# Optimization experiments

Hardware: AMD Instinct MI355X
Metric: run time of the kernel (lower is better)

Reference implementation:

```python
import jax, jax.numpy as jnp
import numpy as np
from jax.scipy.linalg import cho_solve

N = 4096        # num nodes
D = 256         # in_dim == out_dim
NUM_HOPS = 2
R = 32          # subspace_dim
ETA = 0.5
EPS_SUB = 0.5   # eps in coeff = r / (n * eps^2)
LN_EPS = 1e-5


def setup_inputs() -> dict:
    rng = np.random.default_rng(0)
    K = NUM_HOPS + 1
    # sparse-ish binary adjacency mask with self loops
    mask = (rng.random((N, N)) < 0.002).astype(np.float32)
    mask = np.maximum(mask, np.eye(N, dtype=np.float32))
    deg = mask.sum(axis=1, keepdims=True)
    A = (mask / deg).astype(np.float32)          # row-stochastic propagation
    L = (np.eye(N, dtype=np.float32) - A)        # normalized Laplacian
    H = rng.standard_normal((N, D)).astype(np.float32)
    # orthonormal subspace bases per hop, as in __init__ (QR of randn)
    U = np.stack([np.linalg.qr(rng.standard_normal((D, R)))[0][:, :R] for _ in range(K)]).astype(np.float32)
    lambda_laps = np.full((K,), 0.1, dtype=np.float32)
    hop_weights = np.full((K,), 1.0 / K, dtype=np.float32)
    threshold = np.full((D,), 0.05, dtype=np.float32)
    gamma = np.ones((D,), dtype=np.float32)
    beta = np.zeros((D,), dtype=np.float32)
    return {
        "H": jnp.asarray(H), "A": jnp.asarray(A), "adj_mask": jnp.asarray(mask),
        "L": jnp.asarray(L), "U": jnp.asarray(U),
        "lambda_laps": jnp.asarray(lambda_laps), "hop_weights": jnp.asarray(hop_weights),
        "threshold": jnp.asarray(threshold), "gamma": jnp.asarray(gamma), "beta": jnp.asarray(beta),
    }


def reference(H, A, adj_mask, L, U, lambda_laps, hop_weights, threshold, gamma, beta):
    n, d = H.shape
    r = U.shape[-1]
    # multi-hop propagation
    hops = [H]
    Hk = H
    for _ in range(NUM_HOPS):
        Hk = A @ Hk
        hops.append(Hk)
    w = jax.nn.softmax(hop_weights)
    laps = jax.nn.softplus(lambda_laps)
    coeff = r / (n * EPS_SUB ** 2)
    neg = (1.0 - adj_mask) * -1e9
    I_r = jnp.eye(r, dtype=H.dtype)
    agg = jnp.zeros_like(H)        # accumulates grad_k.T, shape [n, d]
    lap_total = jnp.zeros_like(H)
    for k, H_k in enumerate(hops):
        Uk = U[k]                  # [d, r]
        Zk = Uk.T @ H_k.T          # [r, n]
        M = I_r + coeff * (Zk @ Zk.T)              # [r, r], SPD
        Lc = jnp.linalg.cholesky(M)
        M_inv = cho_solve((Lc, True), I_r)         # cholesky_inverse
        MZ = M_inv @ Zk                            # [r, n]
        scores = Zk.T @ MZ + neg                   # [n, n] masked subspace attention
        alpha = jax.nn.softmax(scores, axis=1)
        grad_k = (Uk @ (MZ @ alpha.T)).T           # [n, d]
        agg = agg + w[k] * grad_k
        lap_total = lap_total + laps[k] * (L @ H_k)
    H_half = H + ETA * agg - ETA * lap_total
    # soft-threshold (proj is None since in_dim == out_dim)
    H_out = jnp.sign(H_half) * jax.nn.relu(jnp.abs(H_half) - threshold[None, :])
    H_out = H_out + H              # residual
    mu = H_out.mean(axis=-1, keepdims=True)
    var = H_out.var(axis=-1, keepdims=True)
    H_out = (H_out - mu) / jnp.sqrt(var + LN_EPS) * gamma + beta
    # orthogonality loss over all (k, l) pairs
    K = U.shape[0]
    orth_loss = jnp.asarray(0.0, dtype=H.dtype)
    for k in range(K):
        for l in range(k, K):
            G = U[k].T @ U[l]
            orth_loss = orth_loss + jnp.sum(((G - I_r) if l == k else G) ** 2)
    lap_smooth = jnp.sum(H_out * (L @ H_out))  # trace(H^T L H)
    return H_out, orth_loss, lap_smooth, jax.lax.stop_gradient(w)
```

## Files before the change

### kernel.cpp

```cpp
#include <hip/hip_runtime.h>
#include <math.h>

#define NN 4096
#define DD 256
#define KK 3
#define RR 32
#define MAXNNZ 128

static constexpr float ETA    = 0.5f;
static constexpr float COEFF  = 0.03125f;
static constexpr float LN_EPSF = 1e-5f;

#define OFF_H1   0
#define OFF_H2   (NN*DD)
#define OFF_H3   (2*NN*DD)
#define OFF_Y    (3*NN*DD)
#define OFF_P    (OFF_Y + KK*NN*RR)
#define OFF_M    (OFF_P + KK*NN*RR)
#define OFF_MINV (OFF_M + KK*RR*RR)
#define OFF_SCAL (OFF_MINV + KK*RR*RR)
#define OFF_NNZ  (OFF_SCAL + 8)
#define OFF_COLS (OFF_NNZ + NN)
#define OFF_VALS (OFF_COLS + NN*MAXNNZ)
#define OFF_PART (OFF_VALS + NN*MAXNNZ)
#define OFF_ORTH (OFF_PART + NN/4)
#define OFF_W    (OFF_ORTH + 8)

__global__ __launch_bounds__(256, 4)
void k_csr_prep(const float* __restrict__ A, int* __restrict__ nnz,
                int* __restrict__ cols, float* __restrict__ vals,
                const float* __restrict__ hw, const float* __restrict__ ll,
                const float* __restrict__ U,
                float* __restrict__ ws, float* __restrict__ out,
                const float* __restrict__ H) {
  int b = blockIdx.x;
  int t = threadIdx.x;
  if (b >= NN/2) {
    int p = b - NN/2;
    if (p == 6) {
      if (t == 0) {
        float m = fmaxf(fmaxf(hw[0], hw[1]), hw[2]);
        float e0 = expf(hw[0]-m), e1 = expf(hw[1]-m), e2 = expf(hw[2]-m);
        float s = e0 + e1 + e2;
        float w0 = e0/s, w1 = e1/s, w2 = e2/s;
        ws[OFF_SCAL+0] = w0; ws[OFF_SCAL+1] = w1; ws[OFF_SCAL+2] = w2;
        for (int k = 0; k < KK; ++k) {
          float x = ll[k];
          ws[OFF_SCAL+3+k] = (x > 20.f) ? x : log1pf(expf(x));
        }
        out[NN*DD + 2] = w0; out[NN*DD + 3] = w1; out[NN*DD + 4] = w2;
      }
      for (int idx = t; idx < KK*RR*RR; idx += 256) {
        int rr2 = idx % (RR*RR);
        ws[OFF_M + idx] = ((rr2 / RR) == (rr2 % RR)) ? 1.f : 0.f;
      }
      return;
    }
    int k = (p < 3) ? 0 : ((p < 5) ? 1 : 2);
    int l = (p < 3) ? p : ((p < 5) ? p - 2 : 2);
    int a0 = t >> 5, bb = t & 31;
    float s0 = 0.f, s1 = 0.f, s2 = 0.f, s3 = 0.f;
    for (int dd = 0; dd < DD; ++dd) {
      float ul = U[(size_t)l*DD*RR + dd*RR + bb];
      const float* uk = U + (size_t)k*DD*RR + dd*RR;
      s0 += uk[a0]      * ul;
      s1 += uk[a0 + 8]  * ul;
      s2 += uk[a0 + 16] * ul;
      s3 += uk[a0 + 24] * ul;
    }
    if (k == l && bb == a0)      s0 -= 1.f;
    if (k == l && bb == a0 + 8)  s1 -= 1.f;
    if (k == l && bb == a0 + 16) s2 -= 1.f;
    if (k == l && bb == a0 + 24) s3 -= 1.f;
    float sq = s0*s0 + s1*s1 + s2*s2 + s3*s3;
    #pragma unroll
    for (int o = 32; o > 0; o >>= 1) sq += __shfl_xor(sq, o, 64);
    __shared__ float red[4];
    if ((t & 63) == 0) red[t >> 6] = sq;
    __syncthreads();
    if (t == 0) ws[OFF_ORTH + p] = red[0] + red[1] + red[2] + red[3];
    return;
  }
  int w = t >> 6, lane = t & 63;
  int r = w >> 1, h2 = w & 1;
  int i = b * 2 + r;
  __shared__ int   cbuf[2][2][MAXNNZ];
  __shared__ float vbuf[2][2][MAXNNZ];
  __shared__ int   csr_c[2][MAXNNZ];
  __shared__ float csr_v[2][MAXNNZ];
  __shared__ int   cnts[4];
  __shared__ int   nnzs[2];
  __shared__ float Hs[2][2][DD];
  const float4* row4 = (const float4*)(A + (size_t)i * NN);
  float4 vv[8];
  #pragma unroll
  for (int it = 0; it < 8; ++it) vv[it] = row4[h2*512 + it*64 + lane];
  unsigned long long lower = lane ? (~0ull >> (64 - lane)) : 0ull;
  int base = 0;
  #pragma unroll
  for (int it = 0; it < 8; ++it) {
    float4 v = vv[it];
    int jb = (h2*512 + it*64 + lane) * 4;
    unsigned long long mx = __ballot(v.x != 0.f);
    unsigned long long my = __ballot(v.y != 0.f);
    unsigned long long mz = __ballot(v.z != 0.f);
    unsigned long long mw = __ballot(v.w != 0.f);
    int before = __popcll(mx & lower) + __popcll(my & lower)
               + __popcll(mz & lower) + __popcll(mw & lower);
    int p0 = base + before;
    int bx = (mx >> lane) & 1, by = (my >> lane) & 1, bz = (mz >> lane) & 1;
    if (v.x != 0.f && p0 < MAXNNZ)  { cbuf[r][h2][p0] = jb;   vbuf[r][h2][p0] = v.x; }
    int p1 = p0 + bx;
    if (v.y != 0.f && p1 < MAXNNZ)  { cbuf[r][h2][p1] = jb+1; vbuf[r][h2][p1] = v.y; }
    int p2 = p1 + by;
    if (v.z != 0.f && p2 < MAXNNZ)  { cbuf[r][h2][p2] = jb+2; vbuf[r][h2][p2] = v.z; }
    int p3 = p2 + bz;
    if (v.w != 0.f && p3 < MAXNNZ)  { cbuf[r][h2][p3] = jb+3; vbuf[r][h2][p3] = v.w; }
    base += __popcll(mx) + __popcll(my) + __popcll(mz) + __popcll(mw);
  }
  if (lane == 0) cnts[w] = base < MAXNNZ ? base : MAXNNZ;
  __syncthreads();
  {
    int rr = t >> 7, e0 = t & 127;
    int ii = b * 2 + rr;
    int n0 = cnts[rr*2], n1 = cnts[rr*2 + 1];
    int n = n0 + n1; if (n > MAXNNZ) n = MAXNNZ;
    int npad = (n + 7) & ~7;
    for (int e = e0; e < npad; e += 128) {
      int c; float v;
      if (e < n) {
        if (e < n0) { c = cbuf[rr][0][e];      v = vbuf[rr][0][e]; }
        else        { c = cbuf[rr][1][e - n0]; v = vbuf[rr][1][e - n0]; }
      } else { c = ii; v = 0.f; }
      cols[ii*MAXNNZ + e] = c;
      vals[ii*MAXNNZ + e] = v;
      csr_c[rr][e] = c;
      csr_v[rr][e] = v;
    }
    if (e0 == 0) { nnz[ii] = n; nnzs[rr] = n; }
  }
  __syncthreads();
  float* H1 = ws + OFF_H1;
  if ((w & 1) == 0) {
    int rI = w >> 1;
    int row = b * 2 + rI;
    int d4 = lane * 4;
    int n2 = nnzs[rI], npad2 = (n2 + 7) & ~7;
    float4 acc = {0.f, 0.f, 0.f, 0.f};
    float4 own = {0.f, 0.f, 0.f, 0.f};
    for (int e0i = 0; e0i < npad2; e0i += 8) {
      int4 c0 = *(const int4*)&csr_c[rI][e0i];
      int4 c1 = *(const int4*)&csr_c[rI][e0i + 4];
      float4 v0 = *(const float4*)&csr_v[rI][e0i];
      float4 v1 = *(const float4*)&csr_v[rI][e0i + 4];
      float4 x0 = *(const float4*)(H + (size_t)c0.x*DD + d4);
      float4 x1 = *(const float4*)(H + (size_t)c0.y*DD + d4);
      float4 x2 = *(const float4*)(H + (size_t)c0.z*DD + d4);
      float4 x3 = *(const float4*)(H + (size_t)c0.w*DD + d4);
      float4 x4 = *(const float4*)(H + (size_t)c1.x*DD + d4);
      float4 x5 = *(const float4*)(H + (size_t)c1.y*DD + d4);
      float4 x6 = *(const float4*)(H + (size_t)c1.z*DD + d4);
      float4 x7 = *(const float4*)(H + (size_t)c1.w*DD + d4);
      if (c0.x == row) own = x0;
      if (c0.y == row) own = x1;
      if (c0.z == row) own = x2;
      if (c0.w == row) own = x3;
      if (c1.x == row) own = x4;
      if (c1.y == row) own = x5;
      if (c1.z == row) own = x6;
      if (c1.w == row) own = x7;
      acc.x += v0.x*x0.x + v0.y*x1.x + v0.z*x2.x + v0.w*x3.x + v1.x*x4.x + v1.y*x5.x + v1.z*x6.x + v1.w*x7.x;
      acc.y += v0.x*x0.y + v0.y*x1.y + v0.z*x2.y + v0.w*x3.y + v1.x*x4.y + v1.y*x5.y + v1.z*x6.y + v1.w*x7.y;
      acc.z += v0.x*x0.z + v0.y*x1.z + v0.z*x2.z + v0.w*x3.z + v1.x*x4.z + v1.y*x5.z + v1.z*x6.z + v1.w*x7.z;
      acc.w += v0.x*x0.w + v0.y*x1.w + v0.z*x2.w + v0.w*x3.w + v1.x*x4.w + v1.y*x5.w + v1.z*x6.w + v1.w*x7.w;
    }
    *(float4*)(H1 + (size_t)row*DD + d4) = acc;
    *(float4*)&Hs[rI][0][d4] = own;
    *(float4*)&Hs[rI][1][d4] = acc;
  }
  __syncthreads();
  {
    int rI = w >> 1;
    int row = b * 2 + rI;
    int useAcc = w & 1;
    const float* Up = U + (size_t)useAcc*DD*RR;
    float* Yp = ws + OFF_Y + (size_t)useAcc*NN*RR;
    int c = lane & 31, h = lane >> 5;
    float part = 0.f;
    #pragma unroll 8
    for (int d = h*128; d < h*128 + 128; ++d) part += Hs[rI][useAcc][d] * Up[d*RR + c];
    part += __shfl_xor(part, 32, 64);
    if (h == 0) Yp[(size_t)row*RR + c] = part;
  }
}

__device__ __forceinline__ void spmv_quad(const float* __restrict__ X, int row, int lane,
                                          const int* __restrict__ nnz,
                                          const int* __restrict__ cols,
                                          const float* __restrict__ vals,
                                          float4& acc, float4& own) {
  int d4 = lane * 4;
  int n = nnz[row];
  int npad = (n + 7) & ~7;
  const int* ci = cols + row*MAXNNZ;
  const float* vi = vals + row*MAXNNZ;
  for (int e0 = 0; e0 < npad; e0 += 8) {
    int4 c0 = *(const int4*)(ci + e0);
    int4 c1 = *(const int4*)(ci + e0 + 4);
    float4 v0 = *(const float4*)(vi + e0);
    float4 v1 = *(const float4*)(vi + e0 + 4);
    float4 x0 = *(const float4*)(X + (size_t)c0.x*DD + d4);
    float4 x1 = *(const float4*)(X + (size_t)c0.y*DD + d4);
    float4 x2 = *(const float4*)(X + (size_t)c0.z*DD + d4);
    float4 x3 = *(const float4*)(X + (size_t)c0.w*DD + d4);
    float4 x4 = *(const float4*)(X + (size_t)c1.x*DD + d4);
    float4 x5 = *(const float4*)(X + (size_t)c1.y*DD + d4);
    float4 x6 = *(const float4*)(X + (size_t)c1.z*DD + d4);
    float4 x7 = *(const float4*)(X + (size_t)c1.w*DD + d4);
    if (c0.x == row) own = x0;
    if (c0.y == row) own = x1;
    if (c0.z == row) own = x2;
    if (c0.w == row) own = x3;
    if (c1.x == row) own = x4;
    if (c1.y == row) own = x5;
    if (c1.z == row) own = x6;
    if (c1.w == row) own = x7;
    acc.x += v0.x*x0.x + v0.y*x1.x + v0.z*x2.x + v0.w*x3.x + v1.x*x4.x + v1.y*x5.x + v1.z*x6.x + v1.w*x7.x;
    acc.y += v0.x*x0.y + v0.y*x1.y + v0.z*x2.y + v0.w*x3.y + v1.x*x4.y + v1.y*x5.y + v1.z*x6.y + v1.w*x7.y;
    acc.z += v0.x*x0.z + v0.y*x1.z + v0.z*x2.z + v0.w*x3.z + v1.x*x4.z + v1.y*x5.z + v1.z*x6.z + v1.w*x7.z;
    acc.w += v0.x*x0.w + v0.y*x1.w + v0.z*x2.w + v0.w*x3.w + v1.x*x4.w + v1.y*x5.w + v1.z*x6.w + v1.w*x7.w;
  }
}

__global__ void k_spmvy(const float* __restrict__ X, float* __restrict__ Hout,
                        const int* __restrict__ nnz, const int* __restrict__ cols,
                        const float* __restrict__ vals,
                        const float* __restrict__ Uo, float* __restrict__ Yo,
                        const float* __restrict__ Un, float* __restrict__ Yn) {
  int t = threadIdx.x;
  int r = t >> 6, lane = t & 63;
  int row = blockIdx.x * 4 + r;
  int d4 = lane * 4;
  float4 acc = {0.f, 0.f, 0.f, 0.f};
  float4 own = {0.f, 0.f, 0.f, 0.f};
  spmv_quad(X, row, lane, nnz, cols, vals, acc, own);
  *(float4*)(Hout + (size_t)row*DD + d4) = acc;
  if (!Uo && !Un) return;
  __shared__ float Hs[4][2][DD];
  *(float4*)&Hs[r][0][d4] = own;
  *(float4*)&Hs[r][1][d4] = acc;
  __syncthreads();
  int c = lane & 31, h = lane >> 5;
  if (Uo) {
    float part = 0.f;
    #pragma unroll 8
    for (int d = h*128; d < h*128 + 128; ++d) part += Hs[r][0][d] * Uo[d*RR + c];
    part += __shfl_xor(part, 32, 64);
    if (h == 0) Yo[(size_t)row*RR + c] = part;
  }
  if (Un) {
    float part = 0.f;
    #pragma unroll 8
    for (int d = h*128; d < h*128 + 128; ++d) part += Hs[r][1][d] * Un[d*RR + c];
    part += __shfl_xor(part, 32, 64);
    if (h == 0) Yn[(size_t)row*RR + c] = part;
  }
}

__global__ __launch_bounds__(1024) void k_gram(const float* __restrict__ Y, float* __restrict__ M) {
  int k = blockIdx.y;
  __shared__ float Ys[128*RR];
  int t = threadIdx.x;
  const float* Yk = Y + (size_t)k*NN*RR + (size_t)blockIdx.x*128*RR;
  for (int idx = t; idx < 128*RR; idx += 1024) Ys[idx] = Yk[idx];
  __syncthreads();
  int a = t >> 5, b = t & 31;
  float s = 0.f;
  for (int i = 0; i < 128; ++i) s += Ys[i*RR + a] * Ys[i*RR + b];
  atomicAdd(&M[k*RR*RR + a*RR + b], COEFF * s);
}

__global__ __launch_bounds__(256) void k_gj(const float* __restrict__ M, float* __restrict__ Minv,
                                            const float* __restrict__ U, float* __restrict__ W) {
  int k = blockIdx.x;
  int g = blockIdx.y;
  int t = threadIdx.x;
  __shared__ float B[RR][2*RR + 1];
  for (int idx = t; idx < RR*2*RR; idx += 256) {
    int r = idx >> 6, c = idx & 63;
    B[r][c] = (c < RR) ? M[k*RR*RR + r*RR + c] : ((c - RR == r) ? 1.f : 0.f);
  }
  __syncthreads();
  if (t < 64) {
    for (int p = 0; p < RR; ++p) {
      float rd = 1.f / B[p][p];
      float pb = B[p][t] * rd;
      float f[RR];
      #pragma unroll
      for (int r = 0; r < RR; ++r) f[r] = B[r][p];
      B[p][t] = pb;
      #pragma unroll
      for (int r = 0; r < RR; ++r) {
        if (r == p) continue;
        B[r][t] -= f[r] * pb;
      }
    }
  }
  __syncthreads();
  if (g == 0)
    for (int idx = t; idx < RR*RR; idx += 256)
      Minv[k*RR*RR + idx] = B[idx >> 5][RR + (idx & 31)];
  for (int e = 0; e < 8; ++e) {
    int idx = t + e*256;
    int d = g*64 + (idx >> 5), rr2 = idx & 31;
    const float* ud = U + (size_t)k*DD*RR + (size_t)d*RR;
    float s = 0.f;
    #pragma unroll
    for (int a = 0; a < RR; ++a) s += ud[a] * B[a][RR + rr2];
    W[(size_t)k*DD*RR + (size_t)d*RR + rr2] = s;
  }
}

__global__ __launch_bounds__(256) void k_attn(const float* __restrict__ Y, const float* __restrict__ Minv,
                       float* __restrict__ P, const int* __restrict__ nnz,
                       const int* __restrict__ cols, const float* __restrict__ vals,
                       const float* __restrict__ H2, float* __restrict__ H3) {
  int k = blockIdx.y;
  int t = threadIdx.x;
  int w = t >> 6, lane = t & 63;
  if (blockIdx.x >= NN/4) {
    if (k != 0) return;
    int row = (blockIdx.x - NN/4) * 4 + w;
    float4 acc = {0.f, 0.f, 0.f, 0.f};
    float4 own;
    spmv_quad(H2, row, lane, nnz, cols, vals, acc, own);
    *(float4*)(H3 + (size_t)row*DD + lane*4) = acc;
    return;
  }
  int i = blockIdx.x * 4 + w;
  const float* Yk = Y + (size_t)k*NN*RR;
  __shared__ float Mi[RR*RR];
  __shared__ float Yi[4][RR];
  __shared__ float qv[4][RR];
  __shared__ float sc[4][MAXNNZ];
  __shared__ float Yc[4][32][RR + 1];
  for (int idx = t; idx < RR*RR; idx += 256) Mi[idx] = Minv[k*RR*RR + idx];
  if (lane < RR) Yi[w][lane] = Yk[(size_t)i*RR + lane];
  sc[w][lane] = -1e30f; sc[w][lane+64] = -1e30f;
  __syncthreads();
  if (lane < RR) {
    float s = 0.f;
    #pragma unroll 8
    for (int a = 0; a < RR; ++a) s += Mi[a*RR + lane] * Yi[w][a];
    qv[w][lane] = s;
  }
  int g = lane >> 2, a4 = lane & 3;
  const float* qq = &qv[w][8*a4];
  float q0 = qq[0], q1 = qq[1], q2 = qq[2], q3 = qq[3];
  float q4 = qq[4], q5 = qq[5], q6 = qq[6], q7 = qq[7];
  int n = nnz[i], npad = (n + 7) & ~7;
  const int* ci = cols + i*MAXNNZ;
  for (int e0 = 0; e0 < npad; e0 += 16) {
    int e = e0 + g;
    int ee = (e < npad) ? e : 0;
    int col = ci[ee];
    const float4* yr = (const float4*)(Yk + (size_t)col*RR + 8*a4);
    float4 y0 = yr[0], y1 = yr[1];
    if (e < 32) {
      *(float4*)&Yc[w][e][8*a4]     = y0;
      *(float4*)&Yc[w][e][8*a4 + 4] = y1;
    }
    float s = y0.x*q0 + y0.y*q1 + y0.z*q2 + y0.w*q3
            + y1.x*q4 + y1.y*q5 + y1.z*q6 + y1.w*q7;
    s += __shfl_xor(s, 1, 64);
    s += __shfl_xor(s, 2, 64);
    if (a4 == 0 && e < npad) sc[w][e] = (e < n) ? s : -1e30f;
  }
  float s0 = sc[w][lane], s1 = sc[w][lane+64];
  float m = fmaxf(s0, s1);
  #pragma unroll
  for (int o = 32; o > 0; o >>= 1) m = fmaxf(m, __shfl_xor(m, o, 64));
  float e0v = expf(s0 - m), e1v = expf(s1 - m);
  sc[w][lane] = e0v; sc[w][lane+64] = e1v;
  float l = e0v + e1v;
  #pragma unroll
  for (int o = 32; o > 0; o >>= 1) l += __shfl_xor(l, o, 64);
  float linv = 1.f / l;
  int c = lane & 31, h = lane >> 5;
  float acc = 0.f;
  int lim = npad < 32 ? npad : 32;
  for (int e = h; e < lim; e += 2) acc += sc[w][e] * Yc[w][e][c];
  for (int e = 32 + h; e < npad; e += 2) acc += sc[w][e] * Yk[(size_t)ci[e]*RR + c];
  acc += __shfl_xor(acc, 32, 64);
  if (lane < RR) P[(size_t)k*NN*RR + (size_t)i*RR + lane] = acc * linv;
}

__global__ void k_epi(const float* __restrict__ H0, const float* __restrict__ ws,
                      const float* __restrict__ thr,
                      const float* __restrict__ gma, const float* __restrict__ bta,
                      float* __restrict__ out) {
  __shared__ float Us[DD][RR+1];
  __shared__ float Ps[8][KK*RR];
  int t = threadIdx.x;
  int ty = t >> 5, tx = t & 31;
  int row0 = blockIdx.x * 8;
  const float* P    = ws + OFF_P;
  const float* scal = ws + OFF_SCAL;
  const float* W    = ws + OFF_W;
  for (int idx = t; idx < 8*KK*RR; idx += 256) {
    int rl = idx / (KK*RR), kr = idx % (KK*RR);
    int k = kr / RR, rr2 = kr % RR;
    Ps[rl][kr] = P[(size_t)k*NN*RR + (size_t)(row0+rl)*RR + rr2];
  }
  float lp0 = scal[3], lp1 = scal[4], lp2 = scal[5];
  float gacc[8];
  #pragma unroll
  for (int j = 0; j < 8; ++j) gacc[j] = 0.f;
  for (int k = 0; k < KK; ++k) {
    __syncthreads();
    for (int idx = t; idx < DD*RR/4; idx += 256) {
      float4 w4 = *(const float4*)(W + (size_t)k*DD*RR + (size_t)idx*4);
      int d = (idx*4) >> 5, c = (idx*4) & 31;
      Us[d][c] = w4.x; Us[d][c+1] = w4.y; Us[d][c+2] = w4.z; Us[d][c+3] = w4.w;
    }
    __syncthreads();
    float wk = scal[k];
    #pragma unroll
    for (int j = 0; j < 8; ++j) {
      int d = tx + 32*j;
      float s = 0.f;
      #pragma unroll
      for (int rr2 = 0; rr2 < RR; ++rr2) s += Ps[ty][k*RR + rr2] * Us[d][rr2];
      gacc[j] += wk * s;
    }
  }
  int i = row0 + ty;
  const float* H1 = ws + OFF_H1;
  const float* H2 = ws + OFF_H2;
  const float* H3 = ws + OFF_H3;
  float v[8]; float sum = 0.f, sumsq = 0.f;
  #pragma unroll
  for (int j = 0; j < 8; ++j) {
    int d = tx + 32*j;
    size_t idx = (size_t)i*DD + d;
    float h0 = H0[idx], h1 = H1[idx], h2 = H2[idx], h3 = H3[idx];
    float lap = lp0*(h0-h1) + lp1*(h1-h2) + lp2*(h2-h3);
    float hf = h0 + ETA*gacc[j] - ETA*lap;
    float a = fabsf(hf) - thr[d];
    float sft = (a > 0.f) ? copysignf(a, hf) : 0.f;
    float x = sft + h0;
    v[j] = x; sum += x; sumsq += x*x;
  }
  #pragma unroll
  for (int o = 16; o > 0; o >>= 1) {
    sum   += __shfl_xor(sum, o, 32);
    sumsq += __shfl_xor(sumsq, o, 32);
  }
  float mu  = sum * (1.f/DD);
  float var = sumsq * (1.f/DD) - mu*mu;
  float inv = rsqrtf(var + LN_EPSF);
  #pragma unroll
  for (int j = 0; j < 8; ++j) {
    int d = tx + 32*j;
    out[(size_t)i*DD + d] = (v[j] - mu) * inv * gma[d] + bta[d];
  }
}

__global__ void k_lapsm(const float* __restrict__ Hout, const int* __restrict__ nnz,
                        const int* __restrict__ cols, const float* __restrict__ vals,
                        float* __restrict__ partial) {
  int t = threadIdx.x;
  int row = blockIdx.x * 4 + (t >> 6);
  int d4 = (t & 63) * 4;
  int n = nnz[row];
  int npad = (n + 7) & ~7;
  const int* ci = cols + row*MAXNNZ;
  const float* vi = vals + row*MAXNNZ;
  float4 acc = {0.f, 0.f, 0.f, 0.f};
  for (int e0 = 0; e0 < npad; e0 += 8) {
    int4 c0 = *(const int4*)(ci + e0);
    int4 c1 = *(const int4*)(ci + e0 + 4);
    float4 v0 = *(const float4*)(vi + e0);
    float4 v1 = *(const float4*)(vi + e0 + 4);
    float4 x0 = *(const float4*)(Hout + (size_t)c0.x*DD + d4);
    float4 x1 = *(const float4*)(Hout + (size_t)c0.y*DD + d4);
    float4 x2 = *(const float4*)(Hout + (size_t)c0.z*DD + d4);
    float4 x3 = *(const float4*)(Hout + (size_t)c0.w*DD + d4);
    float4 x4 = *(const float4*)(Hout + (size_t)c1.x*DD + d4);
    float4 x5 = *(const float4*)(Hout + (size_t)c1.y*DD + d4);
    float4 x6 = *(const float4*)(Hout + (size_t)c1.z*DD + d4);
    float4 x7 = *(const float4*)(Hout + (size_t)c1.w*DD + d4);
    acc.x += v0.x*x0.x + v0.y*x1.x + v0.z*x2.x + v0.w*x3.x + v1.x*x4.x + v1.y*x5.x + v1.z*x6.x + v1.w*x7.x;
    acc.y += v0.x*x0.y + v0.y*x1.y + v0.z*x2.y + v0.w*x3.y + v1.x*x4.y + v1.y*x5.y + v1.z*x6.y + v1.w*x7.y;
    acc.z += v0.x*x0.z + v0.y*x1.z + v0.z*x2.z + v0.w*x3.z + v1.x*x4.z + v1.y*x5.z + v1.z*x6.z + v1.w*x7.z;
    acc.w += v0.x*x0.w + v0.y*x1.w + v0.z*x2.w + v0.w*x3.w + v1.x*x4.w + v1.y*x5.w + v1.z*x6.w + v1.w*x7.w;
  }
  float4 h = *(const float4*)(Hout + (size_t)row*DD + d4);
  float part = h.x*(h.x-acc.x) + h.y*(h.y-acc.y) + h.z*(h.z-acc.z) + h.w*(h.w-acc.w);
  #pragma unroll
  for (int o = 32; o > 0; o >>= 1) part += __shfl_xor(part, o, 64);
  __shared__ float red[4];
  if ((t & 63) == 0) red[t >> 6] = part;
  __syncthreads();
  if (t == 0) partial[blockIdx.x] = red[0] + red[1] + red[2] + red[3];
}

__global__ void k_red(const float* __restrict__ ws, float* __restrict__ out) {
  const float* partial = ws + OFF_PART;
  int t = threadIdx.x;
  float4 p = *(const float4*)(partial + t*4);
  float s = p.x + p.y + p.z + p.w;
  #pragma unroll
  for (int o = 32; o > 0; o >>= 1) s += __shfl_xor(s, o, 64);
  __shared__ float red[4];
  if ((t & 63) == 0) red[t >> 6] = s;
  __syncthreads();
  if (t == 0) {
    out[1] = red[0] + red[1] + red[2] + red[3];
    const float* op = ws + OFF_ORTH;
    out[0] = op[0] + op[1] + op[2] + op[3] + op[4] + op[5];
  }
}

extern "C" void kernel_launch(void* const* d_in, const int* in_sizes, int n_in,
                              void* d_out, int out_size, void* d_ws, size_t ws_size,
                              hipStream_t stream) {
  const float* H   = (const float*)d_in[0];
  const float* A   = (const float*)d_in[1];
  const float* U   = (const float*)d_in[4];
  const float* ll  = (const float*)d_in[5];
  const float* hw  = (const float*)d_in[6];
  const float* thr = (const float*)d_in[7];
  const float* gma = (const float*)d_in[8];
  const float* bta = (const float*)d_in[9];
  float* out = (float*)d_out;
  float* ws  = (float*)d_ws;
  int* nnz   = (int*)(ws + OFF_NNZ);
  int* cols  = (int*)(ws + OFF_COLS);
  float* vals = ws + OFF_VALS;
  float* Y = ws + OFF_Y;

  k_csr_prep<<<NN/2 + 7, 256, 0, stream>>>(A, nnz, cols, vals, hw, ll, U, ws, out, H);
  k_spmvy<<<NN/4, 256, 0, stream>>>(ws + OFF_H1, ws + OFF_H2, nnz, cols, vals,
                                    nullptr, nullptr, U + (size_t)2*DD*RR, Y + (size_t)2*NN*RR);
  dim3 g32(NN/128, KK);
  k_gram<<<g32, 1024, 0, stream>>>(Y, ws + OFF_M);
  dim3 ggj(KK, 4);
  k_gj<<<ggj, 256, 0, stream>>>(ws + OFF_M, ws + OFF_MINV, U, ws + OFF_W);
  dim3 gattn(NN/4 + NN/4, KK);
  k_attn<<<gattn, 256, 0, stream>>>(Y, ws + OFF_MINV, ws + OFF_P, nnz, cols, vals,
                                    ws + OFF_H2, ws + OFF_H3);
  k_epi<<<NN/8, 256, 0, stream>>>(H, ws, thr, gma, bta, out);
  k_lapsm<<<NN/4, 256, 0, stream>>>(out, nnz, cols, vals, ws + OFF_PART);
  k_red<<<1, 256, 0, stream>>>(ws, out + NN*DD);
}
```

Measured before the change: 280.2 us.

## Split first-hop SpMV across both waves and overlap hop-0/1 Gram with SpMV

The first-hop sparse row product in the CSR prep kernel now uses both wave halves, each taking alternate 8-entry chunks, and the partial sums are combined through shared memory. The Gram matrix accumulation for hops 0 and 1 moves into 64 extra blocks of the second SpMV launch, so it runs alongside that kernel. The separate Gram launch now only handles hop 2. This shortens the serial dependency chain and keeps idle waves busy, at the cost of an extra shared-memory reduction and barrier and more shared memory per block.

```diff
diff --git a/kernel.cpp b/kernel.cpp
--- a/kernel.cpp
+++ b/kernel.cpp
@@ -91,6 +91,7 @@
   __shared__ int   cnts[4];
   __shared__ int   nnzs[2];
   __shared__ float Hs[2][2][DD];
+  __shared__ float Hs2[2][2][2][DD];
   const float4* row4 = (const float4*)(A + (size_t)i * NN);
   float4 vv[8];
   #pragma unroll
@@ -140,15 +141,14 @@
     if (e0 == 0) { nnz[ii] = n; nnzs[rr] = n; }
   }
   __syncthreads();
-  float* H1 = ws + OFF_H1;
-  if ((w & 1) == 0) {
-    int rI = w >> 1;
+  {
+    int rI = w >> 1, hf = w & 1;
     int row = b * 2 + rI;
     int d4 = lane * 4;
     int n2 = nnzs[rI], npad2 = (n2 + 7) & ~7;
     float4 acc = {0.f, 0.f, 0.f, 0.f};
     float4 own = {0.f, 0.f, 0.f, 0.f};
-    for (int e0i = 0; e0i < npad2; e0i += 8) {
+    for (int e0i = hf*8; e0i < npad2; e0i += 16) {
       int4 c0 = *(const int4*)&csr_c[rI][e0i];
       int4 c1 = *(const int4*)&csr_c[rI][e0i + 4];
       float4 v0 = *(const float4*)&csr_v[rI][e0i];
@@ -174,9 +174,16 @@
       acc.z += v0.x*x0.z + v0.y*x1.z + v0.z*x2.z + v0.w*x3.z + v1.x*x4.z + v1.y*x5.z + v1.z*x6.z + v1.w*x7.z;
       acc.w += v0.x*x0.w + v0.y*x1.w + v0.z*x2.w + v0.w*x3.w + v1.x*x4.w + v1.y*x5.w + v1.z*x6.w + v1.w*x7.w;
     }
-    *(float4*)(H1 + (size_t)row*DD + d4) = acc;
-    *(float4*)&Hs[rI][0][d4] = own;
-    *(float4*)&Hs[rI][1][d4] = acc;
+    *(float4*)&Hs2[rI][0][hf][d4] = own;
+    *(float4*)&Hs2[rI][1][hf][d4] = acc;
+  }
+  __syncthreads();
+  float* H1 = ws + OFF_H1;
+  for (int idx = t; idx < 2*2*DD; idx += 256) {
+    int rI2 = idx >> 9, j = (idx >> 8) & 1, d = idx & 255;
+    float v2 = Hs2[rI2][j][0][d] + Hs2[rI2][j][1][d];
+    Hs[rI2][j][d] = v2;
+    if (j == 1) H1[(size_t)(b*2 + rI2)*DD + d] = v2;
   }
   __syncthreads();
   {
@@ -236,8 +243,32 @@
                         const int* __restrict__ nnz, const int* __restrict__ cols,
                         const float* __restrict__ vals,
                         const float* __restrict__ Uo, float* __restrict__ Yo,
-                        const float* __restrict__ Un, float* __restrict__ Yn) {
-  int t = threadIdx.x;
+                        const float* __restrict__ Un, float* __restrict__ Yn,
+                        const float* __restrict__ Yg, float* __restrict__ Mg) {
+  int t = threadIdx.x;
+  if (blockIdx.x >= NN/4) {
+    if (!Yg) return;
+    int gb = blockIdx.x - NN/4;
+    int k = gb >> 5, g = gb & 31;
+    __shared__ float Ys[128*RR];
+    const float* Yk = Yg + (size_t)k*NN*RR + (size_t)g*128*RR;
+    for (int idx = t; idx < 128*RR; idx += 256) Ys[idx] = Yk[idx];
+    __syncthreads();
+    int a = t >> 3, b4 = (t & 7) * 4;
+    float s0 = 0.f, s1 = 0.f, s2 = 0.f, s3 = 0.f;
+    for (int i = 0; i < 128; ++i) {
+      float ya = Ys[i*RR + a];
+      s0 += ya * Ys[i*RR + b4];
+      s1 += ya * Ys[i*RR + b4 + 1];
+      s2 += ya * Ys[i*RR + b4 + 2];
+      s3 += ya * Ys[i*RR + b4 + 3];
+    }
+    atomicAdd(&Mg[k*RR*RR + a*RR + b4],     COEFF * s0);
+    atomicAdd(&Mg[k*RR*RR + a*RR + b4 + 1], COEFF * s1);
+    atomicAdd(&Mg[k*RR*RR + a*RR + b4 + 2], COEFF * s2);
+    atomicAdd(&Mg[k*RR*RR + a*RR + b4 + 3], COEFF * s3);
+    return;
+  }
   int r = t >> 6, lane = t & 63;
   int row = blockIdx.x * 4 + r;
   int d4 = lane * 4;
@@ -267,17 +298,16 @@
   }
 }
 
-__global__ __launch_bounds__(1024) void k_gram(const float* __restrict__ Y, float* __restrict__ M) {
-  int k = blockIdx.y;
+__global__ __launch_bounds__(1024) void k_gram(const float* __restrict__ Yk, float* __restrict__ Mk) {
   __shared__ float Ys[128*RR];
   int t = threadIdx.x;
-  const float* Yk = Y + (size_t)k*NN*RR + (size_t)blockIdx.x*128*RR;
-  for (int idx = t; idx < 128*RR; idx += 1024) Ys[idx] = Yk[idx];
+  const float* Yb = Yk + (size_t)blockIdx.x*128*RR;
+  for (int idx = t; idx < 128*RR; idx += 1024) Ys[idx] = Yb[idx];
   __syncthreads();
   int a = t >> 5, b = t & 31;
   float s = 0.f;
   for (int i = 0; i < 128; ++i) s += Ys[i*RR + a] * Ys[i*RR + b];
-  atomicAdd(&M[k*RR*RR + a*RR + b], COEFF * s);
+  atomicAdd(&Mk[a*RR + b], COEFF * s);
 }
 
 __global__ __launch_bounds__(256) void k_gj(const float* __restrict__ M, float* __restrict__ Minv,
@@ -541,10 +571,10 @@
   float* Y = ws + OFF_Y;
 
   k_csr_prep<<<NN/2 + 7, 256, 0, stream>>>(A, nnz, cols, vals, hw, ll, U, ws, out, H);
-  k_spmvy<<<NN/4, 256, 0, stream>>>(ws + OFF_H1, ws + OFF_H2, nnz, cols, vals,
-                                    nullptr, nullptr, U + (size_t)2*DD*RR, Y + (size_t)2*NN*RR);
-  dim3 g32(NN/128, KK);
-  k_gram<<<g32, 1024, 0, stream>>>(Y, ws + OFF_M);
+  k_spmvy<<<NN/4 + 64, 256, 0, stream>>>(ws + OFF_H1, ws + OFF_H2, nnz, cols, vals,
+                                         nullptr, nullptr, U + (size_t)2*DD*RR, Y + (size_t)2*NN*RR,
+                                         Y, ws + OFF_M);
+  k_gram<<<NN/128, 1024, 0, stream>>>(Y + (size_t)2*NN*RR, ws + OFF_M + 2*RR*RR);
   dim3 ggj(KK, 4);
   k_gj<<<ggj, 256, 0, stream>>>(ws + OFF_M, ws + OFF_MINV, U, ws + OFF_W);
   dim3 gattn(NN/4 + NN/4, KK);
```

Result: no change. 281.3 us (+0.4%).
